# Optimization experiments

Hardware: AMD Instinct MI355X
Metric: run time of the kernel (lower is better)

Reference implementation:

```python
import jax, jax.numpy as jnp
import numpy as np

# Config matching init_kwargs
N_SEGMENT = 8
N_GROUP = 8
K = 3            # correlation_neighbor
PAD = K // 2     # 1
BN_EPS = 1e-5


def setup_inputs() -> dict:
    key = jax.random.key(0)
    k1, k2, k3 = jax.random.split(key, 3)
    nt, c, h, w = 64, 256, 56, 56
    x = jax.random.normal(k1, (nt, c, h, w), dtype=jnp.float32)
    # Conv2d(72 -> 144, groups=8, kernel=1): weight [144, 9, 1, 1], bias [144]
    w_conv = jax.random.normal(k2, (144, 9, 1, 1), dtype=jnp.float32) * 0.1
    b_conv = jax.random.normal(k3, (144,), dtype=jnp.float32) * 0.1
    gamma = jnp.ones((c,), dtype=jnp.float32)
    beta = jnp.zeros((c,), dtype=jnp.float32)
    return {"x": x, "w_conv": w_conv, "b_conv": b_conv, "gamma": gamma, "beta": beta}


def reference(x, w_conv, b_conv, gamma, beta):
    nt, c, h, w = x.shape
    G = N_GROUP
    cg = c // G
    nt2 = nt // 2

    # ReplicationPad2d(1)
    xp = jnp.pad(x, ((0, 0), (0, 0), (PAD, PAD), (PAD, PAD)), mode="edge")
    x_even = x[::2]          # [nt2, c, h, w]
    xp_odd = xp[1::2]        # [nt2, c, h+2, w+2]

    # Cost volume: shifted multiply + per-group channel sum, 3x3 offsets
    corrs = []
    for i in range(K):
        for j in range(K):
            corr = x_even * jax.lax.slice(xp_odd, (0, 0, i, j), (nt2, c, i + h, j + w))
            corr = corr.reshape(nt2, G, cg, h, w).sum(axis=2)  # [nt2, G, h, w]
            corrs.append(corr)
    corr_feat = jnp.stack(corrs, axis=1)  # [nt2, 9, G, h, w] (offset outer, group inner)

    # Grouped 1x1 conv (groups=G): contiguous channel split of the [9*G] layout
    cr = corr_feat.reshape(nt2, G, K * K, h, w)               # [nt2, G, 9, h, w]
    wg = w_conv.reshape(G, 2 * K * K, K * K)                  # [G, 18, 9]
    xcorr = jnp.einsum("ngihw,goi->ngohw", cr, wg) + b_conv.reshape(1, G, 2 * K * K, 1, 1)
    # view(nt2, 3, 3, 2*G, h, w)
    xcorr = xcorr.reshape(nt2, K, K, 2 * G, h, w)

    # x_pad viewed as (nt, c_per_group, n_group, H+2, W+2)  (group is inner here!)
    xp2 = xp.reshape(nt, cg, G, h + 2, w + 2)
    xp_e = xp2[::2]   # even frames [nt2, cg, G, h+2, w+2]
    xp_o = xp2[1::2]  # odd frames

    # Weighted re-fusion over the 9 offsets (accumulate to avoid a big stack)
    acc = jnp.zeros((nt2, cg, G, h, w), dtype=x.dtype)
    for i in range(K):
        for j in range(K):
            we = xcorr[:, i, j, 0::2][:, None]  # [nt2, 1, G, h, w]
            wo = xcorr[:, i, j, 1::2][:, None]
            acc = acc + xp_e[:, :, :, i:i + h, j:j + w] * we \
                      + xp_o[:, :, :, i:i + h, j:j + w] * wo
    out = acc.reshape(nt2, c, h, w)  # (cg outer, G inner) flatten matches torch view

    # BatchNorm2d (training-mode batch statistics)
    mean = out.mean(axis=(0, 2, 3), keepdims=True)
    var = out.var(axis=(0, 2, 3), keepdims=True)
    out = (out - mean) * jax.lax.rsqrt(var + BN_EPS)
    out = out * gamma.reshape(1, c, 1, 1) + beta.reshape(1, c, 1, 1)
    return out
```

## Files before the change

kernel.cpp:

```cpp
#include <hip/hip_runtime.h>
#include <cstdint>

#define HW 3136
#define WID 56
#define NBLK 1792

typedef float f4v __attribute__((ext_vector_type(4)));

__device__ __forceinline__ int clampi(int v, int lo, int hi) {
    return v < lo ? lo : (v > hi ? hi : v);
}
__device__ __forceinline__ uint32_t rne16(float f) {
    uint32_t b = __float_as_uint(f);
    return (b + 0x7fffu + ((b >> 16) & 1u)) >> 16;
}
__device__ __forceinline__ float blo(uint32_t u) { return __uint_as_float(u << 16); }
__device__ __forceinline__ float bhi(uint32_t u) { return __uint_as_float(u & 0xffff0000u); }
__device__ __forceinline__ uint32_t bpermu(int a4, uint32_t v) {
    return (uint32_t)__builtin_amdgcn_ds_bpermute(a4, (int)v);
}
__device__ __forceinline__ float bperm(int a4, float v) {
    return __int_as_float(__builtin_amdgcn_ds_bpermute(a4, __float_as_int(v)));
}
__device__ __forceinline__ void fma2(float2& a, const float2& u, const float2& w) {
    a.x += u.x * w.x; a.y += u.y * w.y;
}

__global__ __launch_bounds__(256) void tf_pack(const float* __restrict__ x,
                                               uint32_t* __restrict__ xb)
{
    const unsigned total4 = 8192u * 784u;
    unsigned i = blockIdx.x * 256u + threadIdx.x;
    const unsigned stride = gridDim.x * 256u;
    for (; i < total4; i += stride) {
        const unsigned p4 = i / 784u;
        const unsigned i4 = i - p4 * 784u;
        const unsigned pair = p4 >> 8;
        const size_t eoff = ((size_t)pair * 512 + (p4 & 255u)) * HW + i4 * 4;
        const f4v e = __builtin_nontemporal_load((const f4v*)(x + eoff));
        const f4v o = __builtin_nontemporal_load((const f4v*)(x + eoff + (size_t)256 * HW));
        uint4 u;
        u.x = (rne16(o.x) << 16) | rne16(e.x);
        u.y = (rne16(o.y) << 16) | rne16(e.y);
        u.z = (rne16(o.z) << 16) | rne16(e.z);
        u.w = (rne16(o.w) << 16) | rne16(e.w);
        *(uint4*)(xb + (size_t)p4 * HW + i4 * 4) = u;
    }
}

__global__ __launch_bounds__(256, 2) void tf_fused_bf(
    const uint32_t* __restrict__ xb, const float* __restrict__ wconv,
    const float* __restrict__ bconv, float* __restrict__ out)
{
    __shared__ float CP[2 * 9 * 56];
    __shared__ float CR[72 * 56];

    const int d = blockIdx.x;
    const int logical = (d & 7) * 224 + (d >> 3);
    const int n  = logical / 56;
    const int r0 = logical % 56;
    const int t = threadIdx.x;
    const int su = __builtin_amdgcn_readfirstlane(t >> 6);
    const int lane = t & 63;
    const bool act = lane < WID;
    const int px = act ? lane : 55;

    const uint32_t* xq = xb + (size_t)n * 256 * HW;

    const int am = clampi(lane - 1, 0, 55) * 4;
    const int ap = clampi(lane + 1, 0, 55) * 4;

    const int rb0 = clampi(r0 - 1, 0, 55) * WID + px;
    const int rb1 = r0 * WID + px;
    const int rb2 = clampi(r0 + 1, 0, 55) * WID + px;

    for (int g = 0; g < 8; ++g) {
        float crg[9];
        #pragma unroll
        for (int i = 0; i < 9; ++i) crg[i] = 0.f;

        #pragma unroll
        for (int sub = 0; sub < 4; ++sub) {
            const int ch0 = (g * 4 + sub) * 8 + 2 * su;
            #pragma unroll
            for (int c = 0; c < 2; ++c) {
                const uint32_t* base = xq + (size_t)(ch0 + c) * HW;
                const uint32_t u0 = base[rb0], u1 = base[rb1], u2 = base[rb2];
                const float e = blo(u1);
                {   const uint32_t um = bpermu(am, u0), up = bpermu(ap, u0);
                    crg[0] += e * bhi(um); crg[1] += e * bhi(u0); crg[2] += e * bhi(up); }
                {   const uint32_t um = bpermu(am, u1), up = bpermu(ap, u1);
                    crg[3] += e * bhi(um); crg[4] += e * bhi(u1); crg[5] += e * bhi(up); }
                {   const uint32_t um = bpermu(am, u2), up = bpermu(ap, u2);
                    crg[6] += e * bhi(um); crg[7] += e * bhi(u2); crg[8] += e * bhi(up); }
            }
        }
        if (su < 2 && act) {
            #pragma unroll
            for (int ij = 0; ij < 9; ++ij) CP[(su * 9 + ij) * 56 + px] = crg[ij];
        }
        __syncthreads();
        if (su >= 2 && act) {
            const int sl = su - 2;
            #pragma unroll
            for (int ij = 0; ij < 9; ++ij) CP[(sl * 9 + ij) * 56 + px] += crg[ij];
        }
        __syncthreads();
        if (su == 0 && act) {
            #pragma unroll
            for (int ij = 0; ij < 9; ++ij)
                CR[(ij * 8 + g) * 56 + px] =
                    CP[(0 * 9 + ij) * 56 + px] + CP[(1 * 9 + ij) * 56 + px];
        }
        __syncthreads();
    }

    float Wv[9][4];
    #pragma unroll
    for (int ij = 0; ij < 9; ++ij)
        #pragma unroll
        for (int j = 0; j < 4; ++j) {
            const int f = ij * 16 + 4 * su + j;
            const int a = f / 18;
            float w = bconv[f];
            #pragma unroll
            for (int b = 0; b < 9; ++b)
                w += CR[(a * 9 + b) * 56 + px] * wconv[f * 9 + b];
            Wv[ij][j] = w;
        }

    float* ob = out + (size_t)n * 256 * HW + r0 * WID;

    #pragma unroll 2
    for (int q = 0; q < 32; ++q) {
        const int ch0 = q * 8 + 2 * su;
        float a0 = 0.f, a1 = 0.f;
        #pragma unroll
        for (int c = 0; c < 2; ++c) {
            const uint32_t* base = xq + (size_t)(ch0 + c) * HW;
            const uint32_t u0 = base[rb0], u1 = base[rb1], u2 = base[rb2];
            float acc = 0.f;
            {   const uint32_t um = bpermu(am, u0), up = bpermu(ap, u0);
                acc += blo(um) * Wv[0][2 * c] + bhi(um) * Wv[0][2 * c + 1];
                acc += blo(u0) * Wv[1][2 * c] + bhi(u0) * Wv[1][2 * c + 1];
                acc += blo(up) * Wv[2][2 * c] + bhi(up) * Wv[2][2 * c + 1]; }
            {   const uint32_t um = bpermu(am, u1), up = bpermu(ap, u1);
                acc += blo(um) * Wv[3][2 * c] + bhi(um) * Wv[3][2 * c + 1];
                acc += blo(u1) * Wv[4][2 * c] + bhi(u1) * Wv[4][2 * c + 1];
                acc += blo(up) * Wv[5][2 * c] + bhi(up) * Wv[5][2 * c + 1]; }
            {   const uint32_t um = bpermu(am, u2), up = bpermu(ap, u2);
                acc += blo(um) * Wv[6][2 * c] + bhi(um) * Wv[6][2 * c + 1];
                acc += blo(u2) * Wv[7][2 * c] + bhi(u2) * Wv[7][2 * c + 1];
                acc += blo(up) * Wv[8][2 * c] + bhi(up) * Wv[8][2 * c + 1]; }
            if (c == 0) a0 = acc; else a1 = acc;
        }
        if (act) {
            ob[(size_t)ch0 * HW + px] = a0;
            ob[(size_t)(ch0 + 1) * HW + px] = a1;
        }
    }
}

__global__ __launch_bounds__(256, 2) void tf_fused_f32(
    const float* __restrict__ x, const float* __restrict__ wconv,
    const float* __restrict__ bconv, float* __restrict__ out)
{
    __shared__ float2 CP[2 * 9 * 28];
    __shared__ float  CR[72 * 56];

    const int d = blockIdx.x;
    const int logical = (d & 7) * 224 + (d >> 3);
    const int n  = logical / 56;
    const int r0 = logical % 56;
    const int t = threadIdx.x;
    const int wv = t >> 6;
    const int l = t & 63;
    const int sub = l >> 5;
    const int s8 = wv * 2 + sub;
    const int qd0 = l & 31;
    const bool act = qd0 < 28;
    const int qd = act ? qd0 : 27;

    const float* xe = x + (size_t)(2 * n) * 256 * HW;
    const float* xo = xe + (size_t)256 * HW;

    const int am = ((qd0 == 0) ? l : (l - 1)) * 4;
    const int ap = ((qd0 >= 27) ? l : (l + 1)) * 4;
    const bool le = (qd0 == 0);
    const bool re = (qd0 >= 27);

    int rb[3];
    #pragma unroll
    for (int di = 0; di < 3; ++di) rb[di] = clampi(r0 + di - 1, 0, 55) * WID + qd * 2;
    const int rc = r0 * WID + qd * 2;

#define MKTAPS2(v, Tm, Tp)                                  \
    {                                                       \
        const float lwp = bperm(am, (v).y);                 \
        const float rwp = bperm(ap, (v).x);                 \
        Tm = make_float2(le ? (v).x : lwp, (v).x);          \
        Tp = make_float2((v).y, re ? (v).y : rwp);          \
    }

    for (int g = 0; g < 8; ++g) {
        const int ch0 = g * 32 + 4 * s8;
        const float* pe = xe + (size_t)ch0 * HW;
        const float* po = xo + (size_t)ch0 * HW;
        float2 crg[9];
        #pragma unroll
        for (int i = 0; i < 9; ++i) crg[i] = make_float2(0.f, 0.f);
        #pragma unroll
        for (int c = 0; c < 4; ++c) {
            const float2 E = *(const float2*)(pe + (size_t)c * HW + rc);
            #pragma unroll
            for (int di = 0; di < 3; ++di) {
                const float2 O = *(const float2*)(po + (size_t)c * HW + rb[di]);
                float2 Tm, Tp;
                MKTAPS2(O, Tm, Tp)
                fma2(crg[di * 3 + 0], E, Tm);
                fma2(crg[di * 3 + 1], E, O);
                fma2(crg[di * 3 + 2], E, Tp);
            }
        }
        #pragma unroll
        for (int ij = 0; ij < 9; ++ij) {
            crg[ij].x += __shfl_xor(crg[ij].x, 32);
            crg[ij].y += __shfl_xor(crg[ij].y, 32);
        }
        if (wv < 2 && sub == 0 && act) {
            #pragma unroll
            for (int ij = 0; ij < 9; ++ij) CP[(wv * 9 + ij) * 28 + qd] = crg[ij];
        }
        __syncthreads();
        if (wv >= 2 && sub == 0 && act) {
            const int sl = wv - 2;
            #pragma unroll
            for (int ij = 0; ij < 9; ++ij) {
                float2 v = CP[(sl * 9 + ij) * 28 + qd];
                v.x += crg[ij].x; v.y += crg[ij].y;
                CP[(sl * 9 + ij) * 28 + qd] = v;
            }
        }
        __syncthreads();
        if (wv == 0 && sub == 0 && act) {
            #pragma unroll
            for (int ij = 0; ij < 9; ++ij) {
                const float2 v0 = CP[(0 * 9 + ij) * 28 + qd];
                const float2 v1 = CP[(1 * 9 + ij) * 28 + qd];
                float2 v;
                v.x = v0.x + v1.x; v.y = v0.y + v1.y;
                *(float2*)(CR + (ij * 8 + g) * 56 + qd * 2) = v;
            }
        }
        __syncthreads();
    }

    float2 We[9], Wo[9];
    #pragma unroll
    for (int ij = 0; ij < 9; ++ij) {
        const int fe = ij * 16 + 2 * s8;
        const int a = fe / 18;
        const float be = bconv[fe], bo = bconv[fe + 1];
        float2 we = make_float2(be, be);
        float2 wo = make_float2(bo, bo);
        #pragma unroll
        for (int b = 0; b < 9; ++b) {
            const float2 c2 = *(const float2*)(CR + (a * 9 + b) * 56 + qd * 2);
            const float wce = wconv[fe * 9 + b];
            const float wco = wconv[fe * 9 + 9 + b];
            we.x += c2.x * wce; we.y += c2.y * wce;
            wo.x += c2.x * wco; wo.y += c2.y * wco;
        }
        We[ij] = we; Wo[ij] = wo;
    }

    float* ob = out + (size_t)n * 256 * HW + r0 * WID + qd * 2;
    #pragma unroll 2
    for (int k = 0; k < 32; ++k) {
        const int ch = k * 8 + s8;
        const float* pe = xe + (size_t)ch * HW;
        const float* po = xo + (size_t)ch * HW;
        float2 acc = make_float2(0.f, 0.f);
        #pragma unroll
        for (int di = 0; di < 3; ++di) {
            const float2 Ev = *(const float2*)(pe + rb[di]);
            const float2 Ov = *(const float2*)(po + rb[di]);
            float2 TEm, TEp, TOm, TOp;
            MKTAPS2(Ev, TEm, TEp)
            MKTAPS2(Ov, TOm, TOp)
            fma2(acc, TEm, We[di * 3 + 0]); fma2(acc, TOm, Wo[di * 3 + 0]);
            fma2(acc, Ev,  We[di * 3 + 1]); fma2(acc, Ov,  Wo[di * 3 + 1]);
            fma2(acc, TEp, We[di * 3 + 2]); fma2(acc, TOp, Wo[di * 3 + 2]);
        }
        if (act) *(float2*)(ob + (size_t)ch * HW) = acc;
    }
#undef MKTAPS2
}

__global__ void tf_stats_part(const float* __restrict__ out,
                              float* __restrict__ ps, float* __restrict__ pq)
{
    const int ch = blockIdx.x >> 3;
    const int sl = blockIdx.x & 7;
    const int t = threadIdx.x;

    float s = 0.f, q = 0.f;
    #pragma unroll
    for (int k = 0; k < 4; ++k) {
        const float4* p = (const float4*)(out + ((size_t)(4 * sl + k) * 256 + ch) * HW);
        for (int i = t; i < 784; i += 256) {
            const float4 v = p[i];
            s += v.x + v.y + v.z + v.w;
            q += v.x * v.x + v.y * v.y + v.z * v.z + v.w * v.w;
        }
    }
    #pragma unroll
    for (int o = 32; o >= 1; o >>= 1) {
        s += __shfl_xor(s, o);
        q += __shfl_xor(q, o);
    }
    __shared__ float rs[4], rq[4];
    if ((t & 63) == 0) { rs[t >> 6] = s; rq[t >> 6] = q; }
    __syncthreads();
    if (t == 0) {
        ps[blockIdx.x] = rs[0] + rs[1] + rs[2] + rs[3];
        pq[blockIdx.x] = rq[0] + rq[1] + rq[2] + rq[3];
    }
}

__global__ void tf_stats_fin(const float* __restrict__ ps, const float* __restrict__ pq,
                             const float* __restrict__ gamma, const float* __restrict__ beta,
                             float* __restrict__ AB)
{
    const int ch = threadIdx.x;
    float s = 0.f, q = 0.f;
    #pragma unroll
    for (int sl = 0; sl < 8; ++sl) {
        s += ps[ch * 8 + sl];
        q += pq[ch * 8 + sl];
    }
    const float inv = 1.f / 100352.f;
    const float mean = s * inv;
    const float var = q * inv - mean * mean;
    const float rstd = rsqrtf(var + 1e-5f);
    const float A = gamma[ch] * rstd;
    AB[ch] = A;
    AB[256 + ch] = beta[ch] - mean * A;
}

__global__ void tf_norm(float* __restrict__ out, const float* __restrict__ AB)
{
    const unsigned total4 = 32u * 256u * 784u;
    unsigned i = blockIdx.x * 256u + threadIdx.x;
    const unsigned stride = gridDim.x * 256u;
    float4* o4 = (float4*)out;
    for (; i < total4; i += stride) {
        const unsigned ch = (i / 784u) & 255u;
        const float A = AB[ch], B = AB[256 + ch];
        float4 v = o4[i];
        v.x = v.x * A + B;
        v.y = v.y * A + B;
        v.z = v.z * A + B;
        v.w = v.w * A + B;
        o4[i] = v;
    }
}

extern "C" void kernel_launch(void* const* d_in, const int* in_sizes, int n_in,
                              void* d_out, int out_size, void* d_ws, size_t ws_size,
                              hipStream_t stream) {
    const float* x     = (const float*)d_in[0];
    const float* wconv = (const float*)d_in[1];
    const float* bconv = (const float*)d_in[2];
    const float* gamma = (const float*)d_in[3];
    const float* beta  = (const float*)d_in[4];
    float* out = (float*)d_out;

    float* ps = (float*)d_ws;
    float* pq = ps + 2048;
    float* AB = pq + 2048;
    uint32_t* xbuf = (uint32_t*)((uint8_t*)d_ws + 32768);
    const size_t need = 32768 + (size_t)32 * 256 * HW * 4;

    if (ws_size >= need) {
        tf_pack<<<4096, 256, 0, stream>>>(x, xbuf);
        tf_fused_bf<<<NBLK, 256, 0, stream>>>(xbuf, wconv, bconv, out);
    } else {
        tf_fused_f32<<<NBLK, 256, 0, stream>>>(x, wconv, bconv, out);
    }
    tf_stats_part<<<2048, 256, 0, stream>>>(out, ps, pq);
    tf_stats_fin<<<1, 256, 0, stream>>>(ps, pq, gamma, beta, AB);
    tf_norm<<<2048, 256, 0, stream>>>(out, AB);
}
```

Baseline: 203.9 us.

## Store packed bf16 pairs row-major across channels for contiguous per-row reads

The pack kernel now writes the even/odd bf16 pairs as [pair][row][channel][col] instead of [pair][channel][row][col], and the fused kernel indexes that layout. A block working on one output row then reads all 256 channels of its three input rows from three contiguous regions of about 57 KB each, rather than 256 separate rows spread 12.5 KB apart. This is meant to improve cache and TLB locality and DRAM page reuse in the fused kernel. In exchange, the pack kernel's stores become scattered 16-byte writes, which may cost write efficiency.

```diff
diff --git a/kernel.cpp b/kernel.cpp
--- a/kernel.cpp
+++ b/kernel.cpp
@@ -4,6 +4,7 @@
 #define HW 3136
 #define WID 56
 #define NBLK 1792
+#define RSTR 14336
 
 typedef float f4v __attribute__((ext_vector_type(4)));
 
@@ -26,17 +27,21 @@
     a.x += u.x * w.x; a.y += u.y * w.y;
 }
 
-__global__ __launch_bounds__(256) void tf_pack(const float* __restrict__ x,
-                                               uint32_t* __restrict__ xb)
+__global__ __launch_bounds__(256) void tf_pack_t(const float* __restrict__ x,
+                                                 uint32_t* __restrict__ xb)
 {
     const unsigned total4 = 8192u * 784u;
     unsigned i = blockIdx.x * 256u + threadIdx.x;
     const unsigned stride = gridDim.x * 256u;
+    uint4* xb4 = (uint4*)xb;
     for (; i < total4; i += stride) {
         const unsigned p4 = i / 784u;
         const unsigned i4 = i - p4 * 784u;
         const unsigned pair = p4 >> 8;
-        const size_t eoff = ((size_t)pair * 512 + (p4 & 255u)) * HW + i4 * 4;
+        const unsigned ch = p4 & 255u;
+        const unsigned row = i4 / 14u;
+        const unsigned c4 = i4 - row * 14u;
+        const size_t eoff = ((size_t)pair * 512 + ch) * HW + i4 * 4;
         const f4v e = __builtin_nontemporal_load((const f4v*)(x + eoff));
         const f4v o = __builtin_nontemporal_load((const f4v*)(x + eoff + (size_t)256 * HW));
         uint4 u;
@@ -44,11 +49,11 @@
         u.y = (rne16(o.y) << 16) | rne16(e.y);
         u.z = (rne16(o.z) << 16) | rne16(e.z);
         u.w = (rne16(o.w) << 16) | rne16(e.w);
-        *(uint4*)(xb + (size_t)p4 * HW + i4 * 4) = u;
-    }
-}
-
-__global__ __launch_bounds__(256, 2) void tf_fused_bf(
+        xb4[(((size_t)pair * 56 + row) * 256 + ch) * 14 + c4] = u;
+    }
+}
+
+__global__ __launch_bounds__(256, 2) void tf_fused_t(
     const uint32_t* __restrict__ xb, const float* __restrict__ wconv,
     const float* __restrict__ bconv, float* __restrict__ out)
 {
@@ -65,14 +70,14 @@
     const bool act = lane < WID;
     const int px = act ? lane : 55;
 
-    const uint32_t* xq = xb + (size_t)n * 256 * HW;
+    const uint32_t* xq = xb + (size_t)n * 56 * RSTR;
 
     const int am = clampi(lane - 1, 0, 55) * 4;
     const int ap = clampi(lane + 1, 0, 55) * 4;
 
-    const int rb0 = clampi(r0 - 1, 0, 55) * WID + px;
-    const int rb1 = r0 * WID + px;
-    const int rb2 = clampi(r0 + 1, 0, 55) * WID + px;
+    const int Rm = clampi(r0 - 1, 0, 55) * RSTR;
+    const int Rc = r0 * RSTR;
+    const int Rp = clampi(r0 + 1, 0, 55) * RSTR;
 
     for (int g = 0; g < 8; ++g) {
         float crg[9];
@@ -84,8 +89,10 @@
             const int ch0 = (g * 4 + sub) * 8 + 2 * su;
             #pragma unroll
             for (int c = 0; c < 2; ++c) {
-                const uint32_t* base = xq + (size_t)(ch0 + c) * HW;
-                const uint32_t u0 = base[rb0], u1 = base[rb1], u2 = base[rb2];
+                const int co = (ch0 + c) * 56 + px;
+                const uint32_t u0 = xq[Rm + co];
+                const uint32_t u1 = xq[Rc + co];
+                const uint32_t u2 = xq[Rp + co];
                 const float e = blo(u1);
                 {   const uint32_t um = bpermu(am, u0), up = bpermu(ap, u0);
                     crg[0] += e * bhi(um); crg[1] += e * bhi(u0); crg[2] += e * bhi(up); }
@@ -137,8 +144,10 @@
         float a0 = 0.f, a1 = 0.f;
         #pragma unroll
         for (int c = 0; c < 2; ++c) {
-            const uint32_t* base = xq + (size_t)(ch0 + c) * HW;
-            const uint32_t u0 = base[rb0], u1 = base[rb1], u2 = base[rb2];
+            const int co = (ch0 + c) * 56 + px;
+            const uint32_t u0 = xq[Rm + co];
+            const uint32_t u1 = xq[Rc + co];
+            const uint32_t u2 = xq[Rp + co];
             float acc = 0.f;
             {   const uint32_t um = bpermu(am, u0), up = bpermu(ap, u0);
                 acc += blo(um) * Wv[0][2 * c] + bhi(um) * Wv[0][2 * c + 1];
@@ -380,11 +389,11 @@
     float* pq = ps + 2048;
     float* AB = pq + 2048;
     uint32_t* xbuf = (uint32_t*)((uint8_t*)d_ws + 32768);
-    const size_t need = 32768 + (size_t)32 * 256 * HW * 4;
+    const size_t need = 32768 + (size_t)32 * 56 * RSTR * 4;
 
     if (ws_size >= need) {
-        tf_pack<<<4096, 256, 0, stream>>>(x, xbuf);
-        tf_fused_bf<<<NBLK, 256, 0, stream>>>(xbuf, wconv, bconv, out);
+        tf_pack_t<<<4096, 256, 0, stream>>>(x, xbuf);
+        tf_fused_t<<<NBLK, 256, 0, stream>>>(xbuf, wconv, bconv, out);
     } else {
         tf_fused_f32<<<NBLK, 256, 0, stream>>>(x, wconv, bconv, out);
     }
```

Measured after the change: 193.3 us. 1.05x faster.
